# Optimization experiments

Measured on AMD Instinct MI355X. Metric: run time of the kernel, lower is better.

The kernel has to match this reference:

```python
import jax, jax.numpy as jnp
import numpy as np
from jax import lax

B, N = 8, 4096
H = 128          # cfg.net.num_hidden
K = 64           # max_num_neighbors
R1, R2 = 0.2, 0.4
S1, S2 = N // 2, N // 8   # sampling ratios 0.5 and 0.25
OUT = 40


def setup_inputs() -> dict:
    key = jax.random.key(0)
    ks = jax.random.split(key, 32)
    inp = {}
    inp["x"] = jax.random.normal(ks[30], (B, N, 3), jnp.float32)
    inp["pos"] = jax.random.uniform(ks[31], (B, N, 3), jnp.float32)  # unit cube -> radii 0.2/0.4 meaningful
    layers = [("sa1_w1", "sa1_b1", 6, H // 2), ("sa1_w2", "sa1_b2", H // 2, H),
              ("sa2_w1", "sa2_b1", H + 3, H), ("sa2_w2", "sa2_b2", H, 2 * H),
              ("sa3_w1", "sa3_b1", 2 * H + 3, 2 * H), ("sa3_w2", "sa3_b2", 2 * H, 4 * H),
              ("sa3_w3", "sa3_b3", 4 * H, 8 * H),
              ("hd_w1", "hd_b1", 8 * H, 4 * H), ("hd_w2", "hd_b2", 4 * H, 2 * H),
              ("hd_w3", "hd_b3", 2 * H, OUT)]
    for i, (wn, bn, fi, fo) in enumerate(layers):
        inp[wn] = jax.random.normal(ks[i], (fi, fo), jnp.float32) / np.sqrt(fi)
        inp[bn] = jnp.zeros((fo,), jnp.float32)
    return inp


def _mlp(h, layers):
    # Linear+ReLU stack, plain last layer (PyG MLP plain_last=True, eval-mode BN is identity)
    n = len(layers)
    for i, (w, b) in enumerate(layers):
        h = h @ w + b
        if i < n - 1:
            h = jax.nn.relu(h)
    return h


def _fps(p, n_samples):
    # farthest point sampling on one cloud p: [N,3] -> [n_samples] int32
    Np = p.shape[0]

    def step(carry, _):
        min_d, last = carry
        d = jnp.sum((p - p[last]) ** 2, -1)
        min_d = jnp.minimum(min_d, d)
        return (min_d, jnp.argmax(min_d).astype(jnp.int32)), last

    _, idxs = lax.scan(step, (jnp.full((Np,), jnp.inf, p.dtype), jnp.int32(0)),
                       None, length=n_samples)
    return idxs


def _sa(xc, pc, n_samples, r, layers):
    # one SA layer on one cloud: xc [N,C], pc [N,3]
    idx = _fps(pc, n_samples)
    c = pc[idx]                                            # [S,3] centers
    d2 = jnp.sum((c[:, None, :] - pc[None, :, :]) ** 2, -1)  # [S,N]
    d2 = jnp.where(d2 <= r * r, d2, jnp.inf)               # ball query mask
    negd, nbr = lax.top_k(-d2, K)                          # K nearest inside ball
    valid = jnp.isfinite(negd)                             # [S,K]
    feat = jnp.concatenate([xc[nbr], pc[nbr] - c[:, None, :]], -1)  # [S,K,C+3]
    h = _mlp(feat, layers)                                 # [S,K,Cout]
    h = jnp.where(valid[..., None], h, -jnp.inf)
    return jnp.max(h, axis=1), c                           # max-pool over neighborhood


def reference(x, pos, sa1_w1, sa1_b1, sa1_w2, sa1_b2,
              sa2_w1, sa2_b1, sa2_w2, sa2_b2,
              sa3_w1, sa3_b1, sa3_w2, sa3_b2, sa3_w3, sa3_b3,
              hd_w1, hd_b1, hd_w2, hd_b2, hd_w3, hd_b3):
    x1, p1 = jax.vmap(lambda xc, pc: _sa(xc, pc, S1, R1,
                                         [(sa1_w1, sa1_b1), (sa1_w2, sa1_b2)]))(x, pos)
    x2, p2 = jax.vmap(lambda xc, pc: _sa(xc, pc, S2, R2,
                                         [(sa2_w1, sa2_b1), (sa2_w2, sa2_b2)]))(x1, p1)
    # GlobalSAModule: MLP(cat([x,pos])) then global max pool over remaining points
    g = _mlp(jnp.concatenate([x2, p2], -1),
             [(sa3_w1, sa3_b1), (sa3_w2, sa3_b2), (sa3_w3, sa3_b3)])
    g = jnp.max(g, axis=1)                                 # [B, 8H]
    # head MLP (dropout inactive at eval)
    return _mlp(g, [(hd_w1, hd_b1), (hd_w2, hd_b2), (hd_w3, hd_b3)])
```

## Files before the change

### kernel.cpp

```cpp
#include <hip/hip_runtime.h>


constexpr int NBATCH = 8;

typedef float v2f __attribute__((ext_vector_type(2)));

template<int CTRL>
__device__ __forceinline__ float dpp_max_step(float v) {
  int o = __builtin_amdgcn_update_dpp(__float_as_int(v), __float_as_int(v),
                                      CTRL, 0xf, 0xf, false);
  return fmaxf(v, __int_as_float(o));
}
__device__ __forceinline__ float wave_max_bcast(float v) {
  v = dpp_max_step<0x111>(v);
  v = dpp_max_step<0x112>(v);
  v = dpp_max_step<0x114>(v);
  v = dpp_max_step<0x118>(v);
  v = dpp_max_step<0x142>(v);
  v = dpp_max_step<0x143>(v);
  return __int_as_float(__builtin_amdgcn_readlane(__float_as_int(v), 63));
}
template<int CTRL>
__device__ __forceinline__ int dpp_add_step(int v) {
  int o = __builtin_amdgcn_update_dpp(0, v, CTRL, 0xf, 0xf, true);
  return v + o;
}
__device__ __forceinline__ int wave_sum_bcast(int v) {
  v = dpp_add_step<0x111>(v);
  v = dpp_add_step<0x112>(v);
  v = dpp_add_step<0x114>(v);
  v = dpp_add_step<0x118>(v);
  v = dpp_add_step<0x142>(v);
  v = dpp_add_step<0x143>(v);
  return __builtin_amdgcn_readlane(v, 63);
}

#define DIST_PAIR(PX, PY, PZ, MD) { \
  v2f dx = PX - cxv; v2f dy = PY - cyv; v2f dz = PZ - czv; \
  v2f d = (dx * dx + dy * dy) + dz * dz; \
  MD = __builtin_elementwise_min(MD, d); \
  bv2 = __builtin_elementwise_max(bv2, MD); }

__device__ void fps1_one(const float* __restrict__ p, float* __restrict__ cb) {
#pragma clang fp contract(off)
  constexpr int NTH = 512, PT = 8, NW = 8, NSAMP = 2048;
  __shared__ unsigned long long skey[2][NW];
  __shared__ float sxyz[2][NW][3];
  __shared__ float scb[NSAMP * 3];
  const int t = threadIdx.x, lane = t & 63, w = t >> 6;
  const float INF = __builtin_inff();
  v2f px0, px1, px2, px3, py0, py1, py2, py3, pz0, pz1, pz2, pz3;
  v2f md0, md1, md2, md3;
  {
    int jb = t * PT;
    px0 = (v2f){p[(jb+0)*3+0], p[(jb+1)*3+0]};
    py0 = (v2f){p[(jb+0)*3+1], p[(jb+1)*3+1]};
    pz0 = (v2f){p[(jb+0)*3+2], p[(jb+1)*3+2]};
    px1 = (v2f){p[(jb+2)*3+0], p[(jb+3)*3+0]};
    py1 = (v2f){p[(jb+2)*3+1], p[(jb+3)*3+1]};
    pz1 = (v2f){p[(jb+2)*3+2], p[(jb+3)*3+2]};
    px2 = (v2f){p[(jb+4)*3+0], p[(jb+5)*3+0]};
    py2 = (v2f){p[(jb+4)*3+1], p[(jb+5)*3+1]};
    pz2 = (v2f){p[(jb+4)*3+2], p[(jb+5)*3+2]};
    px3 = (v2f){p[(jb+6)*3+0], p[(jb+7)*3+0]};
    py3 = (v2f){p[(jb+6)*3+1], p[(jb+7)*3+1]};
    pz3 = (v2f){p[(jb+6)*3+2], p[(jb+7)*3+2]};
    md0 = (v2f){INF, INF}; md1 = (v2f){INF, INF};
    md2 = (v2f){INF, INF}; md3 = (v2f){INF, INF};
  }
  float cx = p[0], cy = p[1], cz = p[2];
  if (t == 0) { scb[0] = cx; scb[1] = cy; scb[2] = cz; }
  for (int s = 0; s < NSAMP - 1; ++s) {
    v2f cxv = {cx, cx}, cyv = {cy, cy}, czv = {cz, cz};
    v2f bv2 = (v2f){-INF, -INF};
    DIST_PAIR(px0, py0, pz0, md0)
    DIST_PAIR(px1, py1, pz1, md1)
    DIST_PAIR(px2, py2, pz2, md2)
    DIST_PAIR(px3, py3, pz3, md3)
    float bv = fmaxf(bv2.x, bv2.y);
    int bi = 0;
    if (md3.y == bv) bi = 7;
    if (md3.x == bv) bi = 6;
    if (md2.y == bv) bi = 5;
    if (md2.x == bv) bi = 4;
    if (md1.y == bv) bi = 3;
    if (md1.x == bv) bi = 2;
    if (md0.y == bv) bi = 1;
    if (md0.x == bv) bi = 0;
    float wmax = wave_max_bcast(bv);
    unsigned long long ball = __ballot(bv == wmax);
    int fl = __ffsll((long long)ball) - 1;
    int ib = __builtin_amdgcn_readlane(bi, fl);
    int gidx = ((w << 6) + fl) * PT + ib;
    int kk = ib >> 1;
    v2f sx = px0, sy = py0, sz = pz0;
    if (kk == 1) { sx = px1; sy = py1; sz = pz1; }
    if (kk == 2) { sx = px2; sy = py2; sz = pz2; }
    if (kk == 3) { sx = px3; sy = py3; sz = pz3; }
    float wx = (ib & 1) ? sx.y : sx.x;
    float wy = (ib & 1) ? sy.y : sy.x;
    float wz = (ib & 1) ? sz.y : sz.x;
    wx = __int_as_float(__builtin_amdgcn_readlane(__float_as_int(wx), fl));
    wy = __int_as_float(__builtin_amdgcn_readlane(__float_as_int(wy), fl));
    wz = __int_as_float(__builtin_amdgcn_readlane(__float_as_int(wz), fl));
    if (lane == 0) {
      skey[s & 1][w] = (((unsigned long long)(unsigned)__float_as_int(wmax)) << 32)
                       | (unsigned)(~gidx);
      sxyz[s & 1][w][0] = wx; sxyz[s & 1][w][1] = wy; sxyz[s & 1][w][2] = wz;
    }
    __syncthreads();
    unsigned long long best = skey[s & 1][0];
    float nx = sxyz[s & 1][0][0], ny = sxyz[s & 1][0][1], nz = sxyz[s & 1][0][2];
#pragma unroll
    for (int q = 1; q < NW; q++) {
      unsigned long long k2 = skey[s & 1][q];
      bool gt = k2 > best;
      best = gt ? k2 : best;
      nx = gt ? sxyz[s & 1][q][0] : nx;
      ny = gt ? sxyz[s & 1][q][1] : ny;
      nz = gt ? sxyz[s & 1][q][2] : nz;
    }
    cx = nx; cy = ny; cz = nz;
    if (t == 0) { scb[(s + 1) * 3 + 0] = cx; scb[(s + 1) * 3 + 1] = cy;
                  scb[(s + 1) * 3 + 2] = cz; }
  }
  __syncthreads();
  for (int i = t; i < NSAMP * 3; i += NTH) cb[i] = scb[i];
}

__device__ void fps2_one(const float* __restrict__ p, float* __restrict__ cb) {
#pragma clang fp contract(off)
  constexpr int NTH = 512, PT = 4, NW = 8, NSAMP = 512;
  __shared__ unsigned long long skey2[2][NW];
  __shared__ float sxyz2[2][NW][3];
  __shared__ float scb2[NSAMP * 3];
  const int t = threadIdx.x, lane = t & 63, w = t >> 6;
  const float INF = __builtin_inff();
  v2f px0, px1, py0, py1, pz0, pz1, md0, md1;
  {
    int jb = t * PT;
    px0 = (v2f){p[(jb+0)*3+0], p[(jb+1)*3+0]};
    py0 = (v2f){p[(jb+0)*3+1], p[(jb+1)*3+1]};
    pz0 = (v2f){p[(jb+0)*3+2], p[(jb+1)*3+2]};
    px1 = (v2f){p[(jb+2)*3+0], p[(jb+3)*3+0]};
    py1 = (v2f){p[(jb+2)*3+1], p[(jb+3)*3+1]};
    pz1 = (v2f){p[(jb+2)*3+2], p[(jb+3)*3+2]};
    md0 = (v2f){INF, INF}; md1 = (v2f){INF, INF};
  }
  float cx = p[0], cy = p[1], cz = p[2];
  if (t == 0) { scb2[0] = cx; scb2[1] = cy; scb2[2] = cz; }
  for (int s = 0; s < NSAMP - 1; ++s) {
    v2f cxv = {cx, cx}, cyv = {cy, cy}, czv = {cz, cz};
    v2f bv2 = (v2f){-INF, -INF};
    DIST_PAIR(px0, py0, pz0, md0)
    DIST_PAIR(px1, py1, pz1, md1)
    float bv = fmaxf(bv2.x, bv2.y);
    int bi = 0;
    if (md1.y == bv) bi = 3;
    if (md1.x == bv) bi = 2;
    if (md0.y == bv) bi = 1;
    if (md0.x == bv) bi = 0;
    float wmax = wave_max_bcast(bv);
    unsigned long long ball = __ballot(bv == wmax);
    int fl = __ffsll((long long)ball) - 1;
    int ib = __builtin_amdgcn_readlane(bi, fl);
    int gidx = ((w << 6) + fl) * PT + ib;
    int kk = ib >> 1;
    v2f sx = px0, sy = py0, sz = pz0;
    if (kk == 1) { sx = px1; sy = py1; sz = pz1; }
    float wx = (ib & 1) ? sx.y : sx.x;
    float wy = (ib & 1) ? sy.y : sy.x;
    float wz = (ib & 1) ? sz.y : sz.x;
    wx = __int_as_float(__builtin_amdgcn_readlane(__float_as_int(wx), fl));
    wy = __int_as_float(__builtin_amdgcn_readlane(__float_as_int(wy), fl));
    wz = __int_as_float(__builtin_amdgcn_readlane(__float_as_int(wz), fl));
    if (lane == 0) {
      skey2[s & 1][w] = (((unsigned long long)(unsigned)__float_as_int(wmax)) << 32)
                        | (unsigned)(~gidx);
      sxyz2[s & 1][w][0] = wx; sxyz2[s & 1][w][1] = wy; sxyz2[s & 1][w][2] = wz;
    }
    __syncthreads();
    unsigned long long best = skey2[s & 1][0];
    float nx = sxyz2[s & 1][0][0], ny = sxyz2[s & 1][0][1], nz = sxyz2[s & 1][0][2];
#pragma unroll
    for (int q = 1; q < NW; q++) {
      unsigned long long k2 = skey2[s & 1][q];
      bool gt = k2 > best;
      best = gt ? k2 : best;
      nx = gt ? sxyz2[s & 1][q][0] : nx;
      ny = gt ? sxyz2[s & 1][q][1] : ny;
      nz = gt ? sxyz2[s & 1][q][2] : nz;
    }
    cx = nx; cy = ny; cz = nz;
    if (t == 0) { scb2[(s + 1) * 3 + 0] = cx; scb2[(s + 1) * 3 + 1] = cy;
                  scb2[(s + 1) * 3 + 2] = cz; }
  }
  __syncthreads();
  for (int i = t; i < NSAMP * 3; i += NTH) cb[i] = scb2[i];
}

template<int NPTS, int SPB, int LCAP, int WPB>
__device__ void ballquery_body(int bb, const float* __restrict__ pts,
    const float* __restrict__ ctr, float rr,
    int* __restrict__ nbr, int* __restrict__ cnt_out) {
#pragma clang fp contract(off)
  constexpr int KREG = LCAP / 64;
  const int gw = bb * WPB + (threadIdx.x >> 6);
  const int lane = threadIdx.x & 63;
  const int b = gw / SPB;
  __shared__ unsigned long long list_[WPB][LCAP];
  unsigned long long* list = list_[threadIdx.x >> 6];
  const float* p = pts + (size_t)b * NPTS * 3;
  const float* c = ctr + (size_t)gw * 3;
  const float cx = c[0], cy = c[1], cz = c[2];
  const unsigned long long lmask = (1ull << lane) - 1ull;
  int cnt = 0;
  for (int j0 = 0; j0 < NPTS; j0 += 64) {
    int j = j0 + lane;
    float dx = p[j * 3 + 0] - cx, dy = p[j * 3 + 1] - cy, dz = p[j * 3 + 2] - cz;
    float d = (dx * dx + dy * dy) + dz * dz;
    bool in = (d <= rr);
    unsigned long long bal = __ballot(in);
    int pos = cnt + __popcll(bal & lmask);
    if (in && pos < LCAP)
      list[pos] = (((unsigned long long)__float_as_uint(d)) << 32) | (unsigned)j;
    cnt += __popcll(bal);
  }
  if (cnt > LCAP) cnt = LCAP;
  __syncthreads();
  int* nbrp = nbr + (size_t)gw * 64;
  const int nr = (cnt + 63) >> 6;
  unsigned long long key[KREG];
#pragma unroll
  for (int r = 0; r < KREG; r++) {
    int slot = r * 64 + lane;
    key[r] = (r < nr && slot < cnt) ? list[slot] : ~0ull;
  }
  if (cnt <= 64) {
    nbrp[lane] = (lane < cnt) ? (int)(unsigned)key[0] : 0;
    if (lane == 0) cnt_out[gw] = cnt;
    return;
  }
  unsigned pref = 0; int cbase = 0;
  for (int bit = 29; bit >= 0; --bit) {
    int cc = 0;
#pragma unroll
    for (int r = 0; r < KREG; r++) if (r < nr) {
      unsigned db = (unsigned)(key[r] >> 32);
      cc += ((db >> bit) == (pref >> bit)) ? 1 : 0;
    }
    cc = wave_sum_bcast(cc);
    if (cbase + cc < 64) { cbase += cc; pref |= (1u << bit); }
  }
  int base = 0;
#pragma unroll
  for (int r = 0; r < KREG; r++) if (r < nr) {
    unsigned db = (unsigned)(key[r] >> 32);
    bool sel = db < pref;
    unsigned long long m = __ballot(sel);
    if (sel) nbrp[base + __popcll(m & lmask)] = (int)(unsigned)key[r];
    base += __popcll(m);
  }
  int need = 64 - base;
  for (int t2 = 0; t2 < need; ++t2) {
    unsigned besti = 0xffffffffu;
#pragma unroll
    for (int r = 0; r < KREG; r++) if (r < nr) {
      if ((unsigned)(key[r] >> 32) == pref) {
        unsigned v = (unsigned)key[r];
        besti = v < besti ? v : besti;
      }
    }
#pragma unroll
    for (int off = 32; off; off >>= 1) {
      unsigned o = __shfl_xor(besti, off, 64);
      besti = o < besti ? o : besti;
    }
    unsigned long long wk = (((unsigned long long)pref) << 32) | besti;
#pragma unroll
    for (int r = 0; r < KREG; r++) if (r < nr && key[r] == wk) key[r] = ~0ull;
    if (lane == 0) nbrp[base + t2] = (int)besti;
  }
  if (lane == 0) cnt_out[gw] = 64;
}

__device__ void q1_body(int bb, const float* __restrict__ x,
    const float* __restrict__ pos, const float* __restrict__ w, float* __restrict__ q) {
  int gw = bb * 8 + (threadIdx.x >> 6), lane = threadIdx.x & 63;
  const float* xr = x + (size_t)gw * 3; const float* pr = pos + (size_t)gw * 3;
  float a = 0.f;
#pragma unroll
  for (int m = 0; m < 3; m++) a = fmaf(xr[m], w[m * 64 + lane], a);
#pragma unroll
  for (int m = 0; m < 3; m++) a = fmaf(pr[m], w[(3 + m) * 64 + lane], a);
  q[(size_t)gw * 64 + lane] = a;
}

__device__ void t1_body(int bb, const float* __restrict__ c1,
    const float* __restrict__ w, const float* __restrict__ b1, float* __restrict__ t) {
  int gw = bb * 8 + (threadIdx.x >> 6), lane = threadIdx.x & 63;
  const float* cr = c1 + (size_t)gw * 3;
  float a = b1[lane];
#pragma unroll
  for (int m = 0; m < 3; m++) a = fmaf(-cr[m], w[(3 + m) * 64 + lane], a);
  t[(size_t)gw * 64 + lane] = a;
}

__device__ void t2_body(int bb, const float* __restrict__ c2,
    const float* __restrict__ w, const float* __restrict__ b1, float* __restrict__ t) {
  int gw = (bb << 2) + (threadIdx.x >> 6), lane = threadIdx.x & 63;
  const float* cr = c2 + (size_t)gw * 3;
  float a0 = b1[lane], a1 = b1[64 + lane];
#pragma unroll
  for (int m = 0; m < 3; m++) {
    a0 = fmaf(-cr[m], w[(128 + m) * 128 + lane], a0);
    a1 = fmaf(-cr[m], w[(128 + m) * 128 + 64 + lane], a1);
  }
  t[(size_t)gw * 128 + lane] = a0;
  t[(size_t)gw * 128 + 64 + lane] = a1;
}

__device__ void concat3_body(int bb, const float* __restrict__ c2, float* __restrict__ xin3) {
  int row = bb * 256 + threadIdx.x;
  if (row < NBATCH * 512) {
    float* o = xin3 + (size_t)row * 272 + 256;
    const float* c = c2 + (size_t)row * 3;
    o[0] = c[0]; o[1] = c[1]; o[2] = c[2];
#pragma unroll
    for (int i = 3; i < 16; i++) o[i] = 0.f;
  }
}

template<int CIN, int COUT, int OSTR, int NPB, int SPB>
__device__ void sa_pool_body(int bb, const float* __restrict__ q,
    const float* __restrict__ t, const int* __restrict__ nbr, const int* __restrict__ cnt,
    const float* __restrict__ w2, const float* __restrict__ b2, float* __restrict__ out) {
  int gw = (bb << 2) + (threadIdx.x >> 6), lane = threadIdx.x & 63;
  int b = gw / SPB;
  int nk = nbr[(size_t)gw * 64 + lane];
  int c = cnt[gw];
  const float* qr = q + ((size_t)b * NPB + nk) * CIN;
  const float* tr = t + (size_t)gw * CIN;
  float h[CIN];
#pragma unroll
  for (int i = 0; i < CIN; i += 4) {
    float4 v = *(const float4*)(qr + i);
    h[i]     = fmaxf(v.x + tr[i], 0.f);
    h[i + 1] = fmaxf(v.y + tr[i + 1], 0.f);
    h[i + 2] = fmaxf(v.z + tr[i + 2], 0.f);
    h[i + 3] = fmaxf(v.w + tr[i + 3], 0.f);
  }
  bool valid = lane < c;
  float* op = out + (size_t)gw * OSTR;
#pragma unroll 1
  for (int nc = 0; nc < COUT; nc += 16) {
    float acc[16];
#pragma unroll
    for (int u = 0; u < 16; u++) acc[u] = b2[nc + u];
#pragma unroll
    for (int i = 0; i < CIN; i++) {
      const float* wr = w2 + (size_t)i * COUT + nc;
#pragma unroll
      for (int u = 0; u < 16; u++) acc[u] = fmaf(h[i], wr[u], acc[u]);
    }
#pragma unroll
    for (int u = 0; u < 16; u++) {
      float v = valid ? acc[u] : -__builtin_inff();
#pragma unroll
      for (int off = 32; off; off >>= 1) v = fmaxf(v, __shfl_xor(v, off, 64));
      acc[u] = v;
    }
    if (lane == 0) {
#pragma unroll
      for (int u = 0; u < 16; u += 4)
        *(float4*)(op + nc + u) = make_float4(acc[u], acc[u + 1], acc[u + 2], acc[u + 3]);
    }
  }
}

__global__ __launch_bounds__(512, 2) void fuse1_kernel(const float* __restrict__ pos,
    const float* __restrict__ x, const float* __restrict__ w11,
    float* __restrict__ c1, float* __restrict__ q1) {
  int bid = blockIdx.x;
  if (bid < 8)
    fps1_one(pos + (size_t)bid * 4096 * 3, c1 + (size_t)bid * 2048 * 3);
  else
    q1_body(bid - 8, x, pos, w11, q1);
}

__global__ __launch_bounds__(512, 2) void fuse2_kernel(const float* __restrict__ pos,
    const float* __restrict__ c1, const float* __restrict__ w11, const float* __restrict__ b11,
    float* __restrict__ c2, int* __restrict__ nbr1, int* __restrict__ cnt1,
    float* __restrict__ t1buf, float rr1) {
  int bid = blockIdx.x;
  if (bid < 8)
    fps2_one(c1 + (size_t)bid * 2048 * 3, c2 + (size_t)bid * 512 * 3);
  else if (bid < 8 + 2048)
    ballquery_body<4096, 2048, 512, 8>(bid - 8, pos, c1, rr1, nbr1, cnt1);
  else
    t1_body(bid - (8 + 2048), c1, w11, b11, t1buf);
}

__global__ __launch_bounds__(256) void fuse3_kernel(const float* __restrict__ q1buf,
    const float* __restrict__ t1buf, const int* __restrict__ nbr1, const int* __restrict__ cnt1,
    const float* __restrict__ w12, const float* __restrict__ b12, float* __restrict__ x1,
    const float* __restrict__ c1, const float* __restrict__ c2, float rr2,
    int* __restrict__ nbr2, int* __restrict__ cnt2,
    const float* __restrict__ w21, const float* __restrict__ b21, float* __restrict__ t2buf,
    float* __restrict__ xin3) {
  int bid = blockIdx.x;
  if (bid < 4096)
    sa_pool_body<64, 128, 128, 4096, 2048>(bid, q1buf, t1buf, nbr1, cnt1, w12, b12, x1);
  else if (bid < 4096 + 1024)
    ballquery_body<2048, 512, 1024, 4>(bid - 4096, c1, c2, rr2, nbr2, cnt2);
  else if (bid < 4096 + 1024 + 1024)
    t2_body(bid - (4096 + 1024), c2, w21, b21, t2buf);
  else
    concat3_body(bid - (4096 + 1024 + 1024), c2, xin3);
}

__global__ __launch_bounds__(256) void q2_kernel(const float* __restrict__ x1,
    const float* __restrict__ p1, const float* __restrict__ w, float* __restrict__ q2) {
  int gw = (blockIdx.x << 2) + (threadIdx.x >> 6), lane = threadIdx.x & 63;
  const float* xr = x1 + (size_t)gw * 128; const float* pr = p1 + (size_t)gw * 3;
  float a0 = 0.f, a1 = 0.f;
#pragma unroll 8
  for (int m = 0; m < 128; m++) {
    float v = xr[m];
    a0 = fmaf(v, w[m * 128 + lane], a0);
    a1 = fmaf(v, w[m * 128 + 64 + lane], a1);
  }
#pragma unroll
  for (int m = 0; m < 3; m++) {
    float v = pr[m];
    a0 = fmaf(v, w[(128 + m) * 128 + lane], a0);
    a1 = fmaf(v, w[(128 + m) * 128 + 64 + lane], a1);
  }
  q2[(size_t)gw * 128 + lane] = a0;
  q2[(size_t)gw * 128 + 64 + lane] = a1;
}

__global__ __launch_bounds__(256) void sa_pool2_kernel(const float* __restrict__ q,
    const float* __restrict__ t, const int* __restrict__ nbr, const int* __restrict__ cnt,
    const float* __restrict__ w2, const float* __restrict__ b2, float* __restrict__ out) {
  sa_pool_body<128, 256, 272, 2048, 512>(blockIdx.x, q, t, nbr, cnt, w2, b2, out);
}

template<int K, int KP, int N, int AST, bool RELU>
__global__ __launch_bounds__(256) void gemm64(const float* __restrict__ A,
    const float* __restrict__ W, const float* __restrict__ bias, float* __restrict__ C) {
  constexpr int NT = N / 64;
  const int bid = blockIdx.x, tid = threadIdx.x;
  const int tm = bid / NT, tn = bid % NT;
  __shared__ __align__(16) float As[16][68];
  __shared__ __align__(16) float Ws[16][68];
  const int arow = tid >> 2, acol = (tid & 3) << 2;
  const int wrow = tid >> 4, wcol = (tid & 15) << 2;
  const int ty = tid >> 4, tx = tid & 15;
  const float* Ap = A + (size_t)(tm * 64 + arow) * AST + acol;
  const float* Wp = W + (size_t)tn * 64 + wcol;
  float acc[4][4] = {};
  for (int k0 = 0; k0 < KP; k0 += 16) {
    float4 av = *(const float4*)(Ap + k0);
    As[acol + 0][arow] = av.x; As[acol + 1][arow] = av.y;
    As[acol + 2][arow] = av.z; As[acol + 3][arow] = av.w;
    int krow = k0 + wrow;
    float4 wv = make_float4(0.f, 0.f, 0.f, 0.f);
    if (krow < K) wv = *(const float4*)(Wp + (size_t)krow * N);
    *(float4*)(&Ws[wrow][wcol]) = wv;
    __syncthreads();
#pragma unroll
    for (int kk = 0; kk < 16; kk++) {
      float4 a4 = *(const float4*)(&As[kk][ty << 2]);
      float4 b4 = *(const float4*)(&Ws[kk][tx << 2]);
      float aa[4] = {a4.x, a4.y, a4.z, a4.w};
      float bb[4] = {b4.x, b4.y, b4.z, b4.w};
#pragma unroll
      for (int mm = 0; mm < 4; mm++)
#pragma unroll
        for (int nn = 0; nn < 4; nn++) acc[mm][nn] = fmaf(aa[mm], bb[nn], acc[mm][nn]);
    }
    __syncthreads();
  }
  const int m0 = tm * 64 + (ty << 2), n0 = tn * 64 + (tx << 2);
#pragma unroll
  for (int mm = 0; mm < 4; mm++) {
    float4 o;
    o.x = acc[mm][0] + bias[n0 + 0];
    o.y = acc[mm][1] + bias[n0 + 1];
    o.z = acc[mm][2] + bias[n0 + 2];
    o.w = acc[mm][3] + bias[n0 + 3];
    if (RELU) { o.x = fmaxf(o.x, 0.f); o.y = fmaxf(o.y, 0.f);
                o.z = fmaxf(o.z, 0.f); o.w = fmaxf(o.w, 0.f); }
    *(float4*)(C + (size_t)(m0 + mm) * N + n0) = o;
  }
}

__global__ void gmax_kernel(const float* __restrict__ h, float* __restrict__ g) {
  int n = blockIdx.x * 256 + threadIdx.x;
  int b = n >> 10, col = n & 1023;
  const float* p = h + ((size_t)b * 512) * 1024 + col;
  float m = -__builtin_inff();
  for (int j = 0; j < 512; j++) m = fmaxf(m, p[(size_t)j * 1024]);
  g[n] = m;
}

__global__ __launch_bounds__(256) void head_kernel(const float* __restrict__ g,
    const float* __restrict__ w1, const float* __restrict__ b1,
    const float* __restrict__ w2, const float* __restrict__ b2,
    const float* __restrict__ w3, const float* __restrict__ b3,
    float* __restrict__ out) {
  int b = blockIdx.x, t = threadIdx.x;
  __shared__ float s1[1024];
  __shared__ float s2[512];
  *(float4*)(s1 + t * 4) = *(const float4*)(g + (size_t)b * 1024 + t * 4);
  __syncthreads();
  {
    float a0 = b1[t], a1 = b1[t + 256];
    for (int i = 0; i < 1024; i++) {
      float v = s1[i];
      a0 = fmaf(v, w1[(size_t)i * 512 + t], a0);
      a1 = fmaf(v, w1[(size_t)i * 512 + t + 256], a1);
    }
    s2[t] = fmaxf(a0, 0.f); s2[t + 256] = fmaxf(a1, 0.f);
  }
  __syncthreads();
  {
    float a = b2[t];
    for (int i = 0; i < 512; i++) a = fmaf(s2[i], w2[(size_t)i * 256 + t], a);
    s1[t] = fmaxf(a, 0.f);
  }
  __syncthreads();
  if (t < 40) {
    float a = b3[t];
    for (int i = 0; i < 256; i++) a = fmaf(s1[i], w3[(size_t)i * 40 + t], a);
    out[(size_t)b * 40 + t] = a;
  }
}

extern "C" void kernel_launch(void* const* d_in, const int* in_sizes, int n_in,
                              void* d_out, int out_size, void* d_ws, size_t ws_size,
                              hipStream_t stream) {
  const float* x   = (const float*)d_in[0];
  const float* pos = (const float*)d_in[1];
  const float* w11 = (const float*)d_in[2];  const float* b11 = (const float*)d_in[3];
  const float* w12 = (const float*)d_in[4];  const float* b12 = (const float*)d_in[5];
  const float* w21 = (const float*)d_in[6];  const float* b21 = (const float*)d_in[7];
  const float* w22 = (const float*)d_in[8];  const float* b22 = (const float*)d_in[9];
  const float* w31 = (const float*)d_in[10]; const float* b31 = (const float*)d_in[11];
  const float* w32 = (const float*)d_in[12]; const float* b32 = (const float*)d_in[13];
  const float* w33 = (const float*)d_in[14]; const float* b33 = (const float*)d_in[15];
  const float* hw1 = (const float*)d_in[16]; const float* hb1 = (const float*)d_in[17];
  const float* hw2 = (const float*)d_in[18]; const float* hb2 = (const float*)d_in[19];
  const float* hw3 = (const float*)d_in[20]; const float* hb3 = (const float*)d_in[21];
  float* out = (float*)d_out;

  char* wsb = (char*)d_ws;
  int*   cnt1 = (int*)(wsb + 81920);
  int*   cnt2 = (int*)(wsb + 147456);
  float* c1   = (float*)(wsb + 163840);
  float* c2   = (float*)(wsb + 360448);
  float* g    = (float*)(wsb + 409600);
  char* big = wsb + 524288;
  int*   nbr1 = (int*)(big + 0);
  float* q1   = (float*)(big + 4194304);
  float* t1   = (float*)(big + 12582912);
  float* h3c  = (float*)(big + 0);
  float* x1   = (float*)(big + 16777216);
  int*   nbr2 = (int*)(big + 25165824);
  float* h3b  = (float*)(big + 16777216);
  float* q2   = (float*)(big + 26214400);
  float* h3a  = (float*)(big + 26214400);
  float* t2   = (float*)(big + 34603008);
  float* xin3 = (float*)(big + 36700160);

  const float RR1 = (float)(0.2 * 0.2);
  const float RR2 = (float)(0.4 * 0.4);

  fuse1_kernel<<<8 + 4096, 512, 0, stream>>>(pos, x, w11, c1, q1);
  fuse2_kernel<<<8 + 2048 + 2048, 512, 0, stream>>>(pos, c1, w11, b11,
                                                    c2, nbr1, cnt1, t1, RR1);
  fuse3_kernel<<<4096 + 1024 + 1024 + 16, 256, 0, stream>>>(q1, t1, nbr1, cnt1,
      w12, b12, x1, c1, c2, RR2, nbr2, cnt2, w21, b21, t2, xin3);
  q2_kernel<<<4096, 256, 0, stream>>>(x1, c1, w21, q2);
  sa_pool2_kernel<<<1024, 256, 0, stream>>>(q2, t2, nbr2, cnt2, w22, b22, xin3);
  gemm64<259, 272, 256, 272, true ><<<256,  256, 0, stream>>>(xin3, w31, b31, h3a);
  gemm64<256, 256, 512, 256, true ><<<512,  256, 0, stream>>>(h3a,  w32, b32, h3b);
  gemm64<512, 512, 1024, 512, false><<<1024, 256, 0, stream>>>(h3b, w33, b33, h3c);
  gmax_kernel<<<32, 256, 0, stream>>>(h3c, g);
  head_kernel<<<NBATCH, 256, 0, stream>>>(g, hw1, hb1, hw2, hb2, hw3, hb3, out);

  (void)in_sizes; (void)n_in; (void)out_size; (void)ws_size;
}
```

Before: 4.116 ms.

## Run FPS with 256-thread blocks and more points per thread, scalar code

The farthest point sampling loops now use 4 waves of 256 threads instead of 8 waves of 512, with each thread holding 16 (FPS1) or 8 (FPS2) points in scalar arrays rather than packed float2 vectors. Fewer waves mean fewer partial results to combine in shared memory per sample, which targets the per-step barrier and reduction cost on this serial critical path. The co-scheduled ball-query, q1 and t1 work is relaunched at 256 threads with twice as many blocks, and the kernels get waves-per-EU hints. In exchange, each thread does twice the distance work and packed-math throughput is lost, which lengthens each step.

```diff
diff --git a/kernel.cpp b/kernel.cpp
--- a/kernel.cpp
+++ b/kernel.cpp
@@ -2,8 +2,6 @@
 
 
 constexpr int NBATCH = 8;
-
-typedef float v2f __attribute__((ext_vector_type(2)));
 
 template<int CTRL>
 __device__ __forceinline__ float dpp_max_step(float v) {
@@ -35,78 +33,56 @@
   return __builtin_amdgcn_readlane(v, 63);
 }
 
-#define DIST_PAIR(PX, PY, PZ, MD) { \
-  v2f dx = PX - cxv; v2f dy = PY - cyv; v2f dz = PZ - czv; \
-  v2f d = (dx * dx + dy * dy) + dz * dz; \
-  MD = __builtin_elementwise_min(MD, d); \
-  bv2 = __builtin_elementwise_max(bv2, MD); }
-
 __device__ void fps1_one(const float* __restrict__ p, float* __restrict__ cb) {
 #pragma clang fp contract(off)
-  constexpr int NTH = 512, PT = 8, NW = 8, NSAMP = 2048;
+  constexpr int NTH = 256, PT = 16, NW = 4, NSAMP = 2048;
   __shared__ unsigned long long skey[2][NW];
   __shared__ float sxyz[2][NW][3];
   __shared__ float scb[NSAMP * 3];
   const int t = threadIdx.x, lane = t & 63, w = t >> 6;
   const float INF = __builtin_inff();
-  v2f px0, px1, px2, px3, py0, py1, py2, py3, pz0, pz1, pz2, pz3;
-  v2f md0, md1, md2, md3;
-  {
-    int jb = t * PT;
-    px0 = (v2f){p[(jb+0)*3+0], p[(jb+1)*3+0]};
-    py0 = (v2f){p[(jb+0)*3+1], p[(jb+1)*3+1]};
-    pz0 = (v2f){p[(jb+0)*3+2], p[(jb+1)*3+2]};
-    px1 = (v2f){p[(jb+2)*3+0], p[(jb+3)*3+0]};
-    py1 = (v2f){p[(jb+2)*3+1], p[(jb+3)*3+1]};
-    pz1 = (v2f){p[(jb+2)*3+2], p[(jb+3)*3+2]};
-    px2 = (v2f){p[(jb+4)*3+0], p[(jb+5)*3+0]};
-    py2 = (v2f){p[(jb+4)*3+1], p[(jb+5)*3+1]};
-    pz2 = (v2f){p[(jb+4)*3+2], p[(jb+5)*3+2]};
-    px3 = (v2f){p[(jb+6)*3+0], p[(jb+7)*3+0]};
-    py3 = (v2f){p[(jb+6)*3+1], p[(jb+7)*3+1]};
-    pz3 = (v2f){p[(jb+6)*3+2], p[(jb+7)*3+2]};
-    md0 = (v2f){INF, INF}; md1 = (v2f){INF, INF};
-    md2 = (v2f){INF, INF}; md3 = (v2f){INF, INF};
+  float px[PT], py[PT], pz[PT], md[PT];
+#pragma unroll
+  for (int i = 0; i < PT; i++) {
+    int j = t * PT + i;
+    px[i] = p[j * 3 + 0]; py[i] = p[j * 3 + 1]; pz[i] = p[j * 3 + 2];
+    md[i] = INF;
   }
   float cx = p[0], cy = p[1], cz = p[2];
   if (t == 0) { scb[0] = cx; scb[1] = cy; scb[2] = cz; }
   for (int s = 0; s < NSAMP - 1; ++s) {
-    v2f cxv = {cx, cx}, cyv = {cy, cy}, czv = {cz, cz};
-    v2f bv2 = (v2f){-INF, -INF};
-    DIST_PAIR(px0, py0, pz0, md0)
-    DIST_PAIR(px1, py1, pz1, md1)
-    DIST_PAIR(px2, py2, pz2, md2)
-    DIST_PAIR(px3, py3, pz3, md3)
-    float bv = fmaxf(bv2.x, bv2.y);
+#pragma unroll
+    for (int i = 0; i < PT; i++) {
+      float dx = px[i] - cx, dy = py[i] - cy, dz = pz[i] - cz;
+      float d = (dx * dx + dy * dy) + dz * dz;
+      md[i] = fminf(md[i], d);
+    }
+    float m8[8];
+#pragma unroll
+    for (int i = 0; i < 8; i++) m8[i] = fmaxf(md[i], md[i + 8]);
+    float m4[4];
+#pragma unroll
+    for (int i = 0; i < 4; i++) m4[i] = fmaxf(m8[i], m8[i + 4]);
+    float bv = fmaxf(fmaxf(m4[0], m4[1]), fmaxf(m4[2], m4[3]));
     int bi = 0;
-    if (md3.y == bv) bi = 7;
-    if (md3.x == bv) bi = 6;
-    if (md2.y == bv) bi = 5;
-    if (md2.x == bv) bi = 4;
-    if (md1.y == bv) bi = 3;
-    if (md1.x == bv) bi = 2;
-    if (md0.y == bv) bi = 1;
-    if (md0.x == bv) bi = 0;
+#pragma unroll
+    for (int i = PT - 1; i >= 1; --i) if (md[i] == bv) bi = i;
     float wmax = wave_max_bcast(bv);
     unsigned long long ball = __ballot(bv == wmax);
     int fl = __ffsll((long long)ball) - 1;
     int ib = __builtin_amdgcn_readlane(bi, fl);
     int gidx = ((w << 6) + fl) * PT + ib;
-    int kk = ib >> 1;
-    v2f sx = px0, sy = py0, sz = pz0;
-    if (kk == 1) { sx = px1; sy = py1; sz = pz1; }
-    if (kk == 2) { sx = px2; sy = py2; sz = pz2; }
-    if (kk == 3) { sx = px3; sy = py3; sz = pz3; }
-    float wx = (ib & 1) ? sx.y : sx.x;
-    float wy = (ib & 1) ? sy.y : sy.x;
-    float wz = (ib & 1) ? sz.y : sz.x;
-    wx = __int_as_float(__builtin_amdgcn_readlane(__float_as_int(wx), fl));
-    wy = __int_as_float(__builtin_amdgcn_readlane(__float_as_int(wy), fl));
-    wz = __int_as_float(__builtin_amdgcn_readlane(__float_as_int(wz), fl));
+    float sx = px[0], sy = py[0], sz = pz[0];
+#pragma unroll
+    for (int k = 1; k < PT; k++)
+      if (ib == k) { sx = px[k]; sy = py[k]; sz = pz[k]; }
+    sx = __int_as_float(__builtin_amdgcn_readlane(__float_as_int(sx), fl));
+    sy = __int_as_float(__builtin_amdgcn_readlane(__float_as_int(sy), fl));
+    sz = __int_as_float(__builtin_amdgcn_readlane(__float_as_int(sz), fl));
     if (lane == 0) {
       skey[s & 1][w] = (((unsigned long long)(unsigned)__float_as_int(wmax)) << 32)
                        | (unsigned)(~gidx);
-      sxyz[s & 1][w][0] = wx; sxyz[s & 1][w][1] = wy; sxyz[s & 1][w][2] = wz;
+      sxyz[s & 1][w][0] = sx; sxyz[s & 1][w][1] = sy; sxyz[s & 1][w][2] = sz;
     }
     __syncthreads();
     unsigned long long best = skey[s & 1][0];
@@ -130,54 +106,51 @@
 
 __device__ void fps2_one(const float* __restrict__ p, float* __restrict__ cb) {
 #pragma clang fp contract(off)
-  constexpr int NTH = 512, PT = 4, NW = 8, NSAMP = 512;
+  constexpr int NTH = 256, PT = 8, NW = 4, NSAMP = 512;
   __shared__ unsigned long long skey2[2][NW];
   __shared__ float sxyz2[2][NW][3];
   __shared__ float scb2[NSAMP * 3];
   const int t = threadIdx.x, lane = t & 63, w = t >> 6;
   const float INF = __builtin_inff();
-  v2f px0, px1, py0, py1, pz0, pz1, md0, md1;
-  {
-    int jb = t * PT;
-    px0 = (v2f){p[(jb+0)*3+0], p[(jb+1)*3+0]};
-    py0 = (v2f){p[(jb+0)*3+1], p[(jb+1)*3+1]};
-    pz0 = (v2f){p[(jb+0)*3+2], p[(jb+1)*3+2]};
-    px1 = (v2f){p[(jb+2)*3+0], p[(jb+3)*3+0]};
-    py1 = (v2f){p[(jb+2)*3+1], p[(jb+3)*3+1]};
-    pz1 = (v2f){p[(jb+2)*3+2], p[(jb+3)*3+2]};
-    md0 = (v2f){INF, INF}; md1 = (v2f){INF, INF};
+  float px[PT], py[PT], pz[PT], md[PT];
+#pragma unroll
+  for (int i = 0; i < PT; i++) {
+    int j = t * PT + i;
+    px[i] = p[j * 3 + 0]; py[i] = p[j * 3 + 1]; pz[i] = p[j * 3 + 2];
+    md[i] = INF;
   }
   float cx = p[0], cy = p[1], cz = p[2];
   if (t == 0) { scb2[0] = cx; scb2[1] = cy; scb2[2] = cz; }
   for (int s = 0; s < NSAMP - 1; ++s) {
-    v2f cxv = {cx, cx}, cyv = {cy, cy}, czv = {cz, cz};
-    v2f bv2 = (v2f){-INF, -INF};
-    DIST_PAIR(px0, py0, pz0, md0)
-    DIST_PAIR(px1, py1, pz1, md1)
-    float bv = fmaxf(bv2.x, bv2.y);
+#pragma unroll
+    for (int i = 0; i < PT; i++) {
+      float dx = px[i] - cx, dy = py[i] - cy, dz = pz[i] - cz;
+      float d = (dx * dx + dy * dy) + dz * dz;
+      md[i] = fminf(md[i], d);
+    }
+    float m4[4];
+#pragma unroll
+    for (int i = 0; i < 4; i++) m4[i] = fmaxf(md[i], md[i + 4]);
+    float bv = fmaxf(fmaxf(m4[0], m4[1]), fmaxf(m4[2], m4[3]));
     int bi = 0;
-    if (md1.y == bv) bi = 3;
-    if (md1.x == bv) bi = 2;
-    if (md0.y == bv) bi = 1;
-    if (md0.x == bv) bi = 0;
+#pragma unroll
+    for (int i = PT - 1; i >= 1; --i) if (md[i] == bv) bi = i;
     float wmax = wave_max_bcast(bv);
     unsigned long long ball = __ballot(bv == wmax);
     int fl = __ffsll((long long)ball) - 1;
     int ib = __builtin_amdgcn_readlane(bi, fl);
     int gidx = ((w << 6) + fl) * PT + ib;
-    int kk = ib >> 1;
-    v2f sx = px0, sy = py0, sz = pz0;
-    if (kk == 1) { sx = px1; sy = py1; sz = pz1; }
-    float wx = (ib & 1) ? sx.y : sx.x;
-    float wy = (ib & 1) ? sy.y : sy.x;
-    float wz = (ib & 1) ? sz.y : sz.x;
-    wx = __int_as_float(__builtin_amdgcn_readlane(__float_as_int(wx), fl));
-    wy = __int_as_float(__builtin_amdgcn_readlane(__float_as_int(wy), fl));
-    wz = __int_as_float(__builtin_amdgcn_readlane(__float_as_int(wz), fl));
+    float sx = px[0], sy = py[0], sz = pz[0];
+#pragma unroll
+    for (int k = 1; k < PT; k++)
+      if (ib == k) { sx = px[k]; sy = py[k]; sz = pz[k]; }
+    sx = __int_as_float(__builtin_amdgcn_readlane(__float_as_int(sx), fl));
+    sy = __int_as_float(__builtin_amdgcn_readlane(__float_as_int(sy), fl));
+    sz = __int_as_float(__builtin_amdgcn_readlane(__float_as_int(sz), fl));
     if (lane == 0) {
       skey2[s & 1][w] = (((unsigned long long)(unsigned)__float_as_int(wmax)) << 32)
                         | (unsigned)(~gidx);
-      sxyz2[s & 1][w][0] = wx; sxyz2[s & 1][w][1] = wy; sxyz2[s & 1][w][2] = wz;
+      sxyz2[s & 1][w][0] = sx; sxyz2[s & 1][w][1] = sy; sxyz2[s & 1][w][2] = sz;
     }
     __syncthreads();
     unsigned long long best = skey2[s & 1][0];
@@ -286,7 +259,7 @@
 
 __device__ void q1_body(int bb, const float* __restrict__ x,
     const float* __restrict__ pos, const float* __restrict__ w, float* __restrict__ q) {
-  int gw = bb * 8 + (threadIdx.x >> 6), lane = threadIdx.x & 63;
+  int gw = (bb << 2) + (threadIdx.x >> 6), lane = threadIdx.x & 63;
   const float* xr = x + (size_t)gw * 3; const float* pr = pos + (size_t)gw * 3;
   float a = 0.f;
 #pragma unroll
@@ -298,7 +271,7 @@
 
 __device__ void t1_body(int bb, const float* __restrict__ c1,
     const float* __restrict__ w, const float* __restrict__ b1, float* __restrict__ t) {
-  int gw = bb * 8 + (threadIdx.x >> 6), lane = threadIdx.x & 63;
+  int gw = (bb << 2) + (threadIdx.x >> 6), lane = threadIdx.x & 63;
   const float* cr = c1 + (size_t)gw * 3;
   float a = b1[lane];
 #pragma unroll
@@ -378,7 +351,9 @@
   }
 }
 
-__global__ __launch_bounds__(512, 2) void fuse1_kernel(const float* __restrict__ pos,
+__global__ __attribute__((amdgpu_flat_work_group_size(256, 256),
+                          amdgpu_waves_per_eu(1, 2)))
+void fuse1_kernel(const float* __restrict__ pos,
     const float* __restrict__ x, const float* __restrict__ w11,
     float* __restrict__ c1, float* __restrict__ q1) {
   int bid = blockIdx.x;
@@ -388,17 +363,19 @@
     q1_body(bid - 8, x, pos, w11, q1);
 }
 
-__global__ __launch_bounds__(512, 2) void fuse2_kernel(const float* __restrict__ pos,
+__global__ __attribute__((amdgpu_flat_work_group_size(256, 256),
+                          amdgpu_waves_per_eu(1, 2)))
+void fuse2_kernel(const float* __restrict__ pos,
     const float* __restrict__ c1, const float* __restrict__ w11, const float* __restrict__ b11,
     float* __restrict__ c2, int* __restrict__ nbr1, int* __restrict__ cnt1,
     float* __restrict__ t1buf, float rr1) {
   int bid = blockIdx.x;
   if (bid < 8)
     fps2_one(c1 + (size_t)bid * 2048 * 3, c2 + (size_t)bid * 512 * 3);
-  else if (bid < 8 + 2048)
-    ballquery_body<4096, 2048, 512, 8>(bid - 8, pos, c1, rr1, nbr1, cnt1);
+  else if (bid < 8 + 4096)
+    ballquery_body<4096, 2048, 512, 4>(bid - 8, pos, c1, rr1, nbr1, cnt1);
   else
-    t1_body(bid - (8 + 2048), c1, w11, b11, t1buf);
+    t1_body(bid - (8 + 4096), c1, w11, b11, t1buf);
 }
 
 __global__ __launch_bounds__(256) void fuse3_kernel(const float* __restrict__ q1buf,
@@ -577,8 +554,8 @@
   const float RR1 = (float)(0.2 * 0.2);
   const float RR2 = (float)(0.4 * 0.4);
 
-  fuse1_kernel<<<8 + 4096, 512, 0, stream>>>(pos, x, w11, c1, q1);
-  fuse2_kernel<<<8 + 2048 + 2048, 512, 0, stream>>>(pos, c1, w11, b11,
+  fuse1_kernel<<<8 + 8192, 256, 0, stream>>>(pos, x, w11, c1, q1);
+  fuse2_kernel<<<8 + 4096 + 4096, 256, 0, stream>>>(pos, c1, w11, b11,
                                                     c2, nbr1, cnt1, t1, RR1);
   fuse3_kernel<<<4096 + 1024 + 1024 + 16, 256, 0, stream>>>(q1, t1, nbr1, cnt1,
       w12, b12, x1, c1, c2, RR2, nbr2, cnt2, w21, b21, t2, xin3);
```

After: 3.616 ms. 1.14x faster.
